# Kernel optimization log

Measured on AMD Instinct MI355X. Metric: run time of the kernel, lower is better.

## Reference

```python
import jax, jax.numpy as jnp
import numpy as np

EMBED_DIM = 1024
N_HEADS = 16
HEAD_DIM = EMBED_DIM // N_HEADS  # 64
ROPE_DIM = 4
N_FREQ = HEAD_DIM // (2 * ROPE_DIM)  # 8 rotary freqs per coordinate axis
ROPE_THETA = 10000.0
FFN_DIM = 4 * EMBED_DIM
N_TOK = 4096
N_SEQ = 8
EPS = 1e-5
NEG_INF = -1e30


def setup_inputs() -> dict:
    key = jax.random.key(0)
    ks = jax.random.split(key, 16)
    s = 0.02
    coords = jax.random.uniform(ks[0], (N_TOK, ROPE_DIM), jnp.float32) * 10.0
    feats = jax.random.normal(ks[1], (N_TOK, EMBED_DIM), jnp.float32)
    interior = jnp.sort(jax.random.randint(ks[2], (N_SEQ - 1,), 1, N_TOK)).astype(jnp.int32)
    cu_seqlens = jnp.concatenate([jnp.zeros((1,), jnp.int32), interior,
                                  jnp.full((1,), N_TOK, jnp.int32)])
    # learnable RoPE inverse frequencies, one bank per coordinate axis
    base = 1.0 / (ROPE_THETA ** (jnp.arange(N_FREQ, dtype=jnp.float32) * 2.0 * ROPE_DIM / HEAD_DIM))
    inv_freq = jnp.tile(base[None, :], (ROPE_DIM, 1))  # [rope_dim, n_freq]
    return {
        "coords": coords,
        "feats": feats,
        "cu_seqlens": cu_seqlens,
        "Wqkv": jax.random.normal(ks[3], (EMBED_DIM, 3 * EMBED_DIM), jnp.float32) * s,
        "bqkv": jnp.zeros((3 * EMBED_DIM,), jnp.float32),
        "Wo": jax.random.normal(ks[4], (EMBED_DIM, EMBED_DIM), jnp.float32) * s,
        "bo": jnp.zeros((EMBED_DIM,), jnp.float32),
        "inv_freq": inv_freq,
        "ln1_g": jnp.ones((EMBED_DIM,), jnp.float32),
        "ln1_b": jnp.zeros((EMBED_DIM,), jnp.float32),
        "W1": jax.random.normal(ks[5], (EMBED_DIM, FFN_DIM), jnp.float32) * s,
        "b1": jnp.zeros((FFN_DIM,), jnp.float32),
        "W2": jax.random.normal(ks[6], (FFN_DIM, EMBED_DIM), jnp.float32) * s,
        "b2": jnp.zeros((EMBED_DIM,), jnp.float32),
        "ln2_g": jnp.ones((EMBED_DIM,), jnp.float32),
        "ln2_b": jnp.zeros((EMBED_DIM,), jnp.float32),
    }


def _layernorm(x, g, b):
    mu = jnp.mean(x, axis=-1, keepdims=True)
    xc = x - mu
    var = jnp.mean(xc * xc, axis=-1, keepdims=True)
    return xc * jax.lax.rsqrt(var + EPS) * g + b


def _block_forward(coords, feats, cu_seqlens, Wqkv, bqkv, Wo, bo, inv_freq,
                   ln1_g, ln1_b, W1, b1, W2, b2, ln2_g, ln2_b):
    N, D = feats.shape
    qkv = (feats @ Wqkv + bqkv).reshape(N, 3, N_HEADS, HEAD_DIM)
    q, k, v = qkv[:, 0], qkv[:, 1], qkv[:, 2]  # each [N, H, hd]

    # multi-dimensional learnable RoPE: each coord axis rotates its freq bank
    ang = jnp.einsum('nd,df->ndf', coords, inv_freq).reshape(N, 1, HEAD_DIM // 2)
    cos, sin = jnp.cos(ang), jnp.sin(ang)

    def rot(x):
        x1, x2 = jnp.split(x, 2, axis=-1)
        return jnp.concatenate([x1 * cos - x2 * sin, x2 * cos + x1 * sin], axis=-1)

    q, k = rot(q), rot(k)

    # varlen block-diagonal attention mask from cu_seqlens
    seg = jnp.searchsorted(cu_seqlens[1:], jnp.arange(N), side='right')
    mask = seg[:, None] == seg[None, :]  # [N, N]

    scores = jnp.einsum('nhd,mhd->hnm', q, k) / np.sqrt(HEAD_DIM).astype(np.float32)
    scores = jnp.where(mask[None, :, :], scores, NEG_INF)
    attn = jax.nn.softmax(scores, axis=-1)
    o = jnp.einsum('hnm,mhd->nhd', attn, v).reshape(N, D) @ Wo + bo

    h = _layernorm(feats + o, ln1_g, ln1_b)
    f = jax.nn.gelu(h @ W1 + b1) @ W2 + b2
    return _layernorm(h + f, ln2_g, ln2_b)


def reference(coords, feats, cu_seqlens, Wqkv, bqkv, Wo, bo, inv_freq,
              ln1_g, ln1_b, W1, b1, W2, b2, ln2_g, ln2_b):
    return _block_forward(coords, feats, cu_seqlens, Wqkv, bqkv, Wo, bo, inv_freq,
                          ln1_g, ln1_b, W1, b1, W2, b2, ln2_g, ln2_b)
```

## Files before the change

### kernel.cpp

```cpp
#include <hip/hip_runtime.h>

#define NTOK 4096
#define EMB  1024
#define NH   16
#define HD   64
#define FFN  4096

typedef __bf16 bf16x8 __attribute__((ext_vector_type(8)));
typedef float  f32x4  __attribute__((ext_vector_type(4)));

#define ASG __attribute__((address_space(1)))
#define ASL __attribute__((address_space(3)))

__device__ __forceinline__ float b2f(unsigned short u) {
    union { unsigned int i; float f; } v; v.i = ((unsigned int)u) << 16; return v.f;
}
__device__ __forceinline__ unsigned short f2b(float f) {
    return __builtin_bit_cast(unsigned short, (__bf16)f);
}
__device__ __forceinline__ float ldf(const void* p, size_t i, int f32) {
    return f32 ? ((const float*)p)[i] : b2f(((const unsigned short*)p)[i]);
}
__device__ __forceinline__ int probe_f32(const void* p) {
    return ((const unsigned int*)p)[0] == 0x3F800000u ? 1 : 0;
}
__device__ __forceinline__ float gelu_f(float x) {
    float z = 0.7978845608028654f * (x + 0.044715f * x * x * x);
    float t = 1.0f - 2.0f / (__expf(2.0f * z) + 1.0f);
    return 0.5f * x * (1.0f + t);
}
__device__ __forceinline__ void gll16(const void* g, void* l) {
    __builtin_amdgcn_global_load_lds((const ASG void*)g, (ASL void*)l, 16, 0, 0);
}

__global__ __launch_bounds__(256) void convert_kernel(
    const void* __restrict__ feats, const void* __restrict__ bqkv,
    const void* __restrict__ bo, const void* __restrict__ b1,
    const void* __restrict__ b2, const void* __restrict__ g1,
    const void* __restrict__ e1, const void* __restrict__ g2,
    const void* __restrict__ e2, const int* __restrict__ cu,
    unsigned short* __restrict__ feats_bf, unsigned short* __restrict__ smalls,
    int* __restrict__ seg, const void* __restrict__ pr) {
    const int f32 = probe_f32(pr);
    int bid = blockIdx.x, tid = threadIdx.x;
    if (bid < 4096) {
        size_t base = (size_t)bid * 1024 + tid * 4;
        union { unsigned short u[4]; int2 v; } U;
#pragma unroll
        for (int i = 0; i < 4; ++i) U.u[i] = f2b(ldf(feats, base + i, f32));
        *reinterpret_cast<int2*>(&feats_bf[base]) = U.v;
    } else if (bid < 4109) {
        int flat = (bid - 4096) * 1024 + tid * 4;
        const void* src; int off;
        if      (flat < 3072)  { src = bqkv; off = 0; }
        else if (flat < 4096)  { src = bo;   off = 3072; }
        else if (flat < 8192)  { src = b1;   off = 4096; }
        else if (flat < 9216)  { src = b2;   off = 8192; }
        else if (flat < 10240) { src = g1;   off = 9216; }
        else if (flat < 11264) { src = e1;   off = 10240; }
        else if (flat < 12288) { src = g2;   off = 11264; }
        else                   { src = e2;   off = 12288; }
        union { unsigned short u[4]; int2 v; } U;
#pragma unroll
        for (int i = 0; i < 4; ++i) U.u[i] = f2b(ldf(src, flat - off + i, f32));
        *reinterpret_cast<int2*>(&smalls[flat]) = U.v;
    } else {
        int n = (bid - 4109) * 256 + tid;
        int s = 0;
#pragma unroll
        for (int i = 1; i <= 8; ++i) s += (cu[i] <= n) ? 1 : 0;
        seg[n] = s;
    }
}

__global__ __launch_bounds__(64) void sched_kernel(
    const int* __restrict__ seg, const int* __restrict__ cu,
    int* __restrict__ perm) {
    __shared__ int w[64];
    int t = threadIdx.x;
    int s0 = seg[t * 64], s1 = seg[t * 64 + 63];
    int kb = cu[s0] & ~63;
    int kend = cu[s1 + 1];
    w[t] = (kend - kb + 63) >> 6;
    __syncthreads();
    int wt = w[t], r = 0;
#pragma unroll
    for (int j = 0; j < 64; ++j) {
        int wj = w[j];
        r += (wj > wt || (wj == wt && j < t)) ? 1 : 0;
    }
    perm[r] = t;
}

__global__ __launch_bounds__(256) void transpose_kernel(
    const void* __restrict__ W, unsigned short* __restrict__ O,
    int K, int N, const void* __restrict__ pr) {
    const int f32 = probe_f32(pr);
    int b = blockIdx.x, tid = threadIdx.x;
    int ntiles = N >> 6;
    int nt = b % ntiles, kt = b / ntiles;
    __shared__ unsigned short T[64][66];
    int cx = (tid & 15) * 4, ry = tid >> 4;
#pragma unroll
    for (int i = 0; i < 4; ++i) {
        int k = kt * 64 + ry + 16 * i;
        size_t base = (size_t)k * N + nt * 64 + cx;
#pragma unroll
        for (int j = 0; j < 4; ++j)
            T[ry + 16 * i][cx + j] = f2b(ldf(W, base + j, f32));
    }
    __syncthreads();
#pragma unroll
    for (int i = 0; i < 4; ++i) {
        int n = nt * 64 + ry + 16 * i;
        union { unsigned short u[4]; int2 v; } U;
#pragma unroll
        for (int j = 0; j < 4; ++j) U.u[j] = T[cx + j][ry + 16 * i];
        *reinterpret_cast<int2*>(&O[(size_t)n * K + kt * 64 + cx]) = U.v;
    }
}

template <int ACT, int OUTEXT, int TN, int SPLITV, int SPLITK>
__global__ __launch_bounds__(256) void gemm128(
    const unsigned short* __restrict__ A, const unsigned short* __restrict__ Bt,
    const unsigned short* __restrict__ bias, void* __restrict__ C,
    void* __restrict__ C2,
    int M, int N, int K, int lda, int ldb, const void* __restrict__ pr) {
    constexpr int NB = TN / 32;
    __shared__ __align__(16) unsigned short As[128 * 64];
    __shared__ __align__(16) unsigned short Bs[TN * 64];
    const int f32 = OUTEXT ? probe_f32(pr) : 0;
    const int tid = threadIdx.x;
    const int wave = tid >> 6, lane = tid & 63;
    const int wy = wave >> 1, wx = wave & 1;
    const int qm = lane & 15, quad = lane >> 4;
    const int z = SPLITK ? (int)blockIdx.z : 0;
    int bx, by;
    if ((gridDim.y & 7) == 0) {
        int lin = blockIdx.y * gridDim.x + blockIdx.x;
        int ypg = gridDim.y >> 3;
        int xcd = lin & 7, s = lin >> 3;
        int sy = s / gridDim.x;
        by = xcd * ypg + sy;
        bx = s - sy * gridDim.x;
    } else { bx = blockIdx.x; by = blockIdx.y; }
    const int m0 = by * 128, n0 = bx * TN;
    const int r = lane >> 3, gl = lane & 7;

    f32x4 acc[4][NB];
#pragma unroll
    for (int i = 0; i < 4; ++i)
#pragma unroll
        for (int j = 0; j < NB; ++j) acc[i][j] = (f32x4){0.f, 0.f, 0.f, 0.f};

    const int koff = SPLITK ? z * K : 0;
    const unsigned short* Ab = A  + (size_t)m0 * lda + koff;
    const unsigned short* Bb = Bt + (size_t)n0 * ldb + koff;

    for (int k0 = 0; k0 < K; k0 += 64) {
#pragma unroll
        for (int i = 0; i < 4; ++i) {
            int cc = wave * 4 + i;
            gll16(Ab + (size_t)(8 * cc + r) * lda + k0 + ((gl ^ r) << 3), &As[cc * 512]);
        }
#pragma unroll
        for (int i = 0; i < NB; ++i) {
            int cc = wave * NB + i;
            gll16(Bb + (size_t)(8 * cc + r) * ldb + k0 + ((gl ^ r) << 3), &Bs[cc * 512]);
        }
        __syncthreads();
#pragma unroll
        for (int h = 0; h < 2; ++h) {
            bf16x8 af[4], bfr[NB];
#pragma unroll
            for (int i = 0; i < 4; ++i) {
                int phys = (((h * 4 + quad) ^ (qm & 7)) << 3);
                af[i] = *reinterpret_cast<const bf16x8*>(&As[(64 * wy + 16 * i + qm) * 64 + phys]);
            }
#pragma unroll
            for (int j = 0; j < NB; ++j) {
                int phys = (((h * 4 + quad) ^ (qm & 7)) << 3);
                bfr[j] = *reinterpret_cast<const bf16x8*>(&Bs[((TN / 2) * wx + 16 * j + qm) * 64 + phys]);
            }
#pragma unroll
            for (int i = 0; i < 4; ++i)
#pragma unroll
                for (int j = 0; j < NB; ++j)
                    acc[i][j] = __builtin_amdgcn_mfma_f32_16x16x32_bf16(af[i], bfr[j], acc[i][j], 0, 0, 0);
        }
        __syncthreads();
    }
#pragma unroll
    for (int j = 0; j < NB; ++j) {
        int col = n0 + (TN / 2) * wx + 16 * j + qm;
        float bv = (SPLITK && z) ? 0.f : b2f(bias[col]);
        if (SPLITV && n0 >= 2048) {
            int d = col - 2048;
#pragma unroll
            for (int i = 0; i < 4; ++i) {
                int rowb = m0 + 64 * wy + 16 * i + quad * 4;
                union { unsigned short u[4]; int2 v; } U;
#pragma unroll
                for (int rr = 0; rr < 4; ++rr) U.u[rr] = f2b(acc[i][j][rr] + bv);
                *reinterpret_cast<int2*>((unsigned short*)C2 + (size_t)d * 4096 + rowb) = U.v;
            }
        } else {
            const int ldc = SPLITV ? 2048 : N;
            void* Cz = (SPLITK && z) ? C2 : C;
#pragma unroll
            for (int i = 0; i < 4; ++i) {
                int rowb = m0 + 64 * wy + 16 * i + quad * 4;
#pragma unroll
                for (int rr = 0; rr < 4; ++rr) {
                    size_t idx = (size_t)(rowb + rr) * ldc + col;
                    float v = acc[i][j][rr] + bv;
                    if (ACT == 1) v = gelu_f(v);
                    if (OUTEXT && f32) ((float*)Cz)[idx] = v;
                    else               ((unsigned short*)Cz)[idx] = f2b(v);
                }
            }
        }
    }
}

__global__ __launch_bounds__(256) void rope_kernel(
    const void* __restrict__ coords, const void* __restrict__ inv_freq,
    unsigned short* __restrict__ qk, const void* __restrict__ pr) {
    const int f32 = probe_f32(pr);
    int n = blockIdx.x, tid = threadIdx.x;
#pragma unroll
    for (int it = 0; it < 2; ++it) {
        int idx = tid + it * 256;
        int hh = idx >> 5, f = idx & 31;
        float c  = ldf(coords, n * 4 + (f >> 3), f32);
        float iv = ldf(inv_freq, f, f32);
        float sn, cs;
        sincosf(c * iv, &sn, &cs);
#pragma unroll
        for (int w = 0; w < 2; ++w) {
            size_t base = (size_t)n * 2048 + (size_t)w * 1024 + hh * 64;
            float scl = w ? 1.0f : 0.125f;
            float x1 = b2f(qk[base + f]);
            float x2 = b2f(qk[base + 32 + f]);
            qk[base + f]      = f2b((x1 * cs - x2 * sn) * scl);
            qk[base + 32 + f] = f2b((x2 * cs + x1 * sn) * scl);
        }
    }
}

__global__ __launch_bounds__(256) void attn_part(
    const unsigned short* __restrict__ qk, const unsigned short* __restrict__ vt,
    const int* __restrict__ seg, const int* __restrict__ cu,
    const int* __restrict__ perm,
    unsigned short* __restrict__ u0, unsigned short* __restrict__ u1,
    unsigned short* __restrict__ u2, float* __restrict__ ml) {
    const int h = blockIdx.x / 3;
    const int piece = blockIdx.x - 3 * h;
    const int t3 = perm[blockIdx.y];
    const int t0 = t3 * 64;
    const int tid  = threadIdx.x;
    const int wave = tid >> 6, lane = tid & 63;
    const int qm = lane & 15, quad = lane >> 4;

    __shared__ __align__(16) unsigned short Ks[2][64][64];
    __shared__ __align__(16) unsigned short Vs[2][80][64];
    __shared__ __align__(16) unsigned short Ps[64][64];
    __shared__ int segq[64], segk[2][64];

    const unsigned short* qrow = qk + (size_t)(t0 + 16 * wave + qm) * 2048 + h * 64;
    bf16x8 af0 = *reinterpret_cast<const bf16x8*>(qrow + quad * 8);
    bf16x8 af1 = *reinterpret_cast<const bf16x8*>(qrow + 32 + quad * 8);

    {
        int rr = tid >> 4, cc = (tid & 15) * 4;
        unsigned short val = (rr == 0) ? (unsigned short)0x3F80 : (unsigned short)0;
#pragma unroll
        for (int b = 0; b < 2; ++b)
#pragma unroll
            for (int j = 0; j < 4; ++j) Vs[b][64 + rr][cc + j] = val;
    }
    if (tid < 64) segq[tid] = seg[t0 + tid];
    __syncthreads();

    const int kbegA = cu[segq[0]] & ~63;
    const int kendT = cu[segq[63] + 1];
    const int nchunks = (kendT - kbegA + 63) >> 6;
    const int third = (nchunks + 2) / 3;
    const int kb = kbegA + piece * third * 64;
    const int ke = min(kendT, kbegA + (piece + 1) * third * 64);

    int sqr[4];
#pragma unroll
    for (int r = 0; r < 4; ++r) sqr[r] = segq[16 * wave + quad * 4 + r];
    const int wsmin = segq[16 * wave];
    const int wsmax = segq[16 * wave + 15];

    float m[4];
    f32x4 o[5];
#pragma unroll
    for (int r = 0; r < 4; ++r) m[r] = -1e30f;
#pragma unroll
    for (int t = 0; t < 5; ++t) o[t] = (f32x4){0.f, 0.f, 0.f, 0.f};

    const int krow = tid >> 2, kdc = (tid & 3) * 16;
    const int k7 = krow & 7;
    const int sw0 = (((tid & 3) * 2) ^ k7) << 3;
    const int sw1 = ((((tid & 3) * 2 + 1)) ^ k7) << 3;
    const int rsw0 = (quad ^ (qm & 7)) << 3;
    const int rsw1 = ((quad + 4) ^ (qm & 7)) << 3;
    int4 kA, kB, vA, vB; int sg;
#define LOAD_CHUNK(KC)                                                                   \
    {                                                                                    \
        const unsigned short* kp = qk + (size_t)((KC) + krow) * 2048 + 1024 + h * 64 + kdc; \
        kA = *reinterpret_cast<const int4*>(kp);                                         \
        kB = *reinterpret_cast<const int4*>(kp + 8);                                     \
        const unsigned short* vp = vt + (size_t)(h * 64 + krow) * 4096 + (KC) + kdc;     \
        vA = *reinterpret_cast<const int4*>(vp);                                         \
        vB = *reinterpret_cast<const int4*>(vp + 8);                                     \
        sg = 127;                                                                        \
        if (tid < 64 && (KC) + tid < ke) sg = seg[(KC) + tid];                           \
    }
#define STORE_CHUNK(B)                                                                   \
    {                                                                                    \
        *reinterpret_cast<int4*>(&Ks[B][krow][sw0]) = kA;                                \
        *reinterpret_cast<int4*>(&Ks[B][krow][sw1]) = kB;                                \
        *reinterpret_cast<int4*>(&Vs[B][krow][sw0]) = vA;                                \
        *reinterpret_cast<int4*>(&Vs[B][krow][sw1]) = vB;                                \
        if (tid < 64) segk[B][tid] = sg;                                                 \
    }

    int cur = 0;
    if (kb < ke) {
        LOAD_CHUNK(kb);
        STORE_CHUNK(0);
    }

    for (int kc = kb; kc < ke; kc += 64) {
        const bool have_next = (kc + 64 < ke);
        if (have_next) LOAD_CHUNK(kc + 64);
        __syncthreads();

        const int skmin = segk[cur][0], skmax = segk[cur][63];
        const bool act = !(skmax < wsmin || skmin > wsmax);

        if (act) {
            f32x4 sc[4];
#pragma unroll
            for (int nb = 0; nb < 4; ++nb) {
                bf16x8 bf0 = *reinterpret_cast<const bf16x8*>(&Ks[cur][16 * nb + qm][rsw0]);
                bf16x8 bf1 = *reinterpret_cast<const bf16x8*>(&Ks[cur][16 * nb + qm][rsw1]);
                f32x4 s = (f32x4){0.f, 0.f, 0.f, 0.f};
                s = __builtin_amdgcn_mfma_f32_16x16x32_bf16(af0, bf0, s, 0, 0, 0);
                s = __builtin_amdgcn_mfma_f32_16x16x32_bf16(af1, bf1, s, 0, 0, 0);
                sc[nb] = s;
            }
            if (!((skmin == skmax) & (wsmin == wsmax))) {
#pragma unroll
                for (int nb = 0; nb < 4; ++nb) {
                    int sk = segk[cur][16 * nb + qm];
#pragma unroll
                    for (int r = 0; r < 4; ++r)
                        sc[nb][r] = (sk == sqr[r]) ? sc[nb][r] : -1e30f;
                }
            }
            float alpha[4];
#pragma unroll
            for (int r = 0; r < 4; ++r) {
                float v = fmaxf(fmaxf(sc[0][r], sc[1][r]), fmaxf(sc[2][r], sc[3][r]));
                v = fmaxf(v, __shfl_xor(v, 1, 64));
                v = fmaxf(v, __shfl_xor(v, 2, 64));
                v = fmaxf(v, __shfl_xor(v, 4, 64));
                v = fmaxf(v, __shfl_xor(v, 8, 64));
                float mn = fmaxf(m[r], v);
                alpha[r] = __expf(m[r] - mn);
                m[r] = mn;
            }
#pragma unroll
            for (int nb = 0; nb < 4; ++nb) {
                int R7 = (quad * 4) & 7;
#pragma unroll
                for (int r = 0; r < 4; ++r) {
                    float p = __expf(sc[nb][r] - m[r]);
                    int row = 16 * wave + quad * 4 + r;
                    int phys = (((2 * nb + (qm >> 3)) ^ ((quad * 4 + r) & 7)) << 3) + (qm & 7);
                    Ps[row][phys] = f2b(p);
                }
                (void)R7;
            }
#pragma unroll
            for (int t = 0; t < 5; ++t)
#pragma unroll
                for (int r = 0; r < 4; ++r) o[t][r] *= alpha[r];

            bf16x8 pa0 = *reinterpret_cast<const bf16x8*>(&Ps[16 * wave + qm][rsw0]);
            bf16x8 pa1 = *reinterpret_cast<const bf16x8*>(&Ps[16 * wave + qm][rsw1]);
#pragma unroll
            for (int dt = 0; dt < 4; ++dt) {
                bf16x8 vb0 = *reinterpret_cast<const bf16x8*>(&Vs[cur][16 * dt + qm][rsw0]);
                bf16x8 vb1 = *reinterpret_cast<const bf16x8*>(&Vs[cur][16 * dt + qm][rsw1]);
                o[dt] = __builtin_amdgcn_mfma_f32_16x16x32_bf16(pa0, vb0, o[dt], 0, 0, 0);
                o[dt] = __builtin_amdgcn_mfma_f32_16x16x32_bf16(pa1, vb1, o[dt], 0, 0, 0);
            }
            {
                bf16x8 vb0 = *reinterpret_cast<const bf16x8*>(&Vs[cur][64 + qm][rsw0]);
                bf16x8 vb1 = *reinterpret_cast<const bf16x8*>(&Vs[cur][64 + qm][rsw1]);
                o[4] = __builtin_amdgcn_mfma_f32_16x16x32_bf16(pa0, vb0, o[4], 0, 0, 0);
                o[4] = __builtin_amdgcn_mfma_f32_16x16x32_bf16(pa1, vb1, o[4], 0, 0, 0);
            }
        }
        if (have_next) {
            STORE_CHUNK(cur ^ 1);
        }
        cur ^= 1;
    }
#undef LOAD_CHUNK
#undef STORE_CHUNK
    unsigned short* dst = (piece == 0) ? u0 : ((piece == 1) ? u1 : u2);
#pragma unroll
    for (int dt = 0; dt < 4; ++dt)
#pragma unroll
        for (int r = 0; r < 4; ++r) {
            int row = t0 + 16 * wave + quad * 4 + r;
            dst[(size_t)row * 1024 + h * 64 + 16 * dt + qm] = f2b(o[dt][r]);
        }
    if (qm == 0) {
        float2* ML = (float2*)ml;
#pragma unroll
        for (int r = 0; r < 4; ++r) {
            int row = t0 + 16 * wave + quad * 4 + r;
            ML[((piece * 16 + h) << 12) + row] = make_float2(m[r], o[4][r]);
        }
    }
}

__global__ __launch_bounds__(256) void combine_kernel(
    const unsigned short* __restrict__ u1, const unsigned short* __restrict__ u2,
    const float* __restrict__ ml, unsigned short* __restrict__ u0out) {
    int n = blockIdx.x, tid = threadIdx.x;
    int d4 = tid * 4, h = tid >> 4;
    const float2* ML = (const float2*)ml;
    float2 p0 = ML[(h << 12) + n];
    float2 p1 = ML[((16 + h) << 12) + n];
    float2 p2 = ML[((32 + h) << 12) + n];
    float M = fmaxf(p0.x, fmaxf(p1.x, p2.x));
    float a0 = __expf(p0.x - M), a1 = __expf(p1.x - M), a2 = __expf(p2.x - M);
    float rcp = 1.0f / (a0 * p0.y + a1 * p1.y + a2 * p2.y);
    size_t ix = (size_t)n * 1024 + d4;
    union { int2 q; unsigned short u[4]; } A, B, Cq, R;
    A.q  = *reinterpret_cast<const int2*>(u0out + ix);
    B.q  = *reinterpret_cast<const int2*>(u1 + ix);
    Cq.q = *reinterpret_cast<const int2*>(u2 + ix);
#pragma unroll
    for (int i = 0; i < 4; ++i)
        R.u[i] = f2b((a0 * b2f(A.u[i]) + a1 * b2f(B.u[i]) + a2 * b2f(Cq.u[i])) * rcp);
    *reinterpret_cast<int2*>(u0out + ix) = R.q;
}

template <int OUTEXT>
__global__ __launch_bounds__(256) void ln3_kernel(
    const unsigned short* __restrict__ x1, const unsigned short* __restrict__ x2a,
    const unsigned short* __restrict__ x2b,
    const unsigned short* __restrict__ g, const unsigned short* __restrict__ b,
    void* __restrict__ out, const void* __restrict__ pr) {
    const int f32 = probe_f32(pr);
    int n = blockIdx.x, tid = threadIdx.x;
    __shared__ float red[8];
    const int d0 = tid * 4;
    const size_t ix0 = (size_t)n * EMB + d0;
    float v[4];
    {
        union { int2 q; unsigned short u[4]; } A, Ba, Bb2;
        A.q   = *reinterpret_cast<const int2*>(&x1[ix0]);
        Ba.q  = *reinterpret_cast<const int2*>(&x2a[ix0]);
        Bb2.q = *reinterpret_cast<const int2*>(&x2b[ix0]);
#pragma unroll
        for (int i = 0; i < 4; ++i)
            v[i] = b2f(A.u[i]) + b2f(Ba.u[i]) + b2f(Bb2.u[i]);
    }
    float s = v[0] + v[1] + v[2] + v[3];
#pragma unroll
    for (int off = 1; off < 64; off <<= 1) s += __shfl_xor(s, off, 64);
    if ((tid & 63) == 0) red[tid >> 6] = s;
    __syncthreads();
    float mu = (red[0] + red[1] + red[2] + red[3]) * (1.0f / 1024.0f);
    float sq = 0.0f;
#pragma unroll
    for (int i = 0; i < 4; ++i) { float c = v[i] - mu; sq += c * c; }
#pragma unroll
    for (int off = 1; off < 64; off <<= 1) sq += __shfl_xor(sq, off, 64);
    if ((tid & 63) == 0) red[4 + (tid >> 6)] = sq;
    __syncthreads();
    float var = (red[4] + red[5] + red[6] + red[7]) * (1.0f / 1024.0f);
    float rcp = rsqrtf(var + 1e-5f);
    union { int2 q; unsigned short u[4]; } G, Bb;
    G.q  = *reinterpret_cast<const int2*>(&g[d0]);
    Bb.q = *reinterpret_cast<const int2*>(&b[d0]);
    if (OUTEXT && f32) {
        float4 R;
        R.x = (v[0] - mu) * rcp * b2f(G.u[0]) + b2f(Bb.u[0]);
        R.y = (v[1] - mu) * rcp * b2f(G.u[1]) + b2f(Bb.u[1]);
        R.z = (v[2] - mu) * rcp * b2f(G.u[2]) + b2f(Bb.u[2]);
        R.w = (v[3] - mu) * rcp * b2f(G.u[3]) + b2f(Bb.u[3]);
        *reinterpret_cast<float4*>((float*)out + ix0) = R;
    } else {
        union { int2 q; unsigned short u[4]; } R;
#pragma unroll
        for (int i = 0; i < 4; ++i)
            R.u[i] = f2b((v[i] - mu) * rcp * b2f(G.u[i]) + b2f(Bb.u[i]));
        *reinterpret_cast<int2*>((unsigned short*)out + ix0) = R.q;
    }
}

extern "C" void kernel_launch(void* const* d_in, const int* in_sizes, int n_in,
                              void* d_out, int out_size, void* d_ws, size_t ws_size,
                              hipStream_t stream) {
    const void* coords   = d_in[0];
    const void* feats    = d_in[1];
    const int*  cu       = (const int*)d_in[2];
    const void* Wqkv     = d_in[3];
    const void* bqkv     = d_in[4];
    const void* Wo       = d_in[5];
    const void* bo       = d_in[6];
    const void* inv_freq = d_in[7];
    const void* ln1_g    = d_in[8];
    const void* ln1_b    = d_in[9];
    const void* W1       = d_in[10];
    const void* b1       = d_in[11];
    const void* W2       = d_in[12];
    const void* b2       = d_in[13];
    const void* ln2_g    = d_in[14];
    const void* ln2_b    = d_in[15];
    const void* pr = ln1_g;

    char* ws = (char*)d_ws;
    int* seg = (int*)ws;
    unsigned short* smalls   = (unsigned short*)(ws + 16384);
    unsigned short* bqkv_bf  = smalls;
    unsigned short* bo_bf    = smalls + 3072;
    unsigned short* b1_bf    = smalls + 4096;
    unsigned short* b2_bf    = smalls + 8192;
    unsigned short* g1_bf    = smalls + 9216;
    unsigned short* e1_bf    = smalls + 10240;
    unsigned short* g2_bf    = smalls + 11264;
    unsigned short* e2_bf    = smalls + 12288;
    int* perm                = (int*)(ws + 49152);
    unsigned short* feats_bf = (unsigned short*)(ws + 65536);
    unsigned short* hbuf     = feats_bf;
    unsigned short* W1_t     = (unsigned short*)(ws + 8454144);
    unsigned short* u1buf    = (unsigned short*)(ws + 16842752);
    unsigned short* Wqkv_t   = (unsigned short*)(ws + 18939904);
    unsigned short* qkbuf    = (unsigned short*)(ws + 25231360);
    unsigned short* vtbuf    = (unsigned short*)(ws + 42008576);
    unsigned short* attn_o   = (unsigned short*)(ws + 50397184);
    unsigned short* Wo_t     = (unsigned short*)(ws + 18939904);
    unsigned short* woP0     = (unsigned short*)(ws + 25231360);
    unsigned short* woP1     = (unsigned short*)(ws + 33619968);
    unsigned short* f1       = (unsigned short*)(ws + 25231360);
    unsigned short* ffP0     = (unsigned short*)(ws + 8454144);
    unsigned short* ffP1     = (unsigned short*)(ws + 16842752);
    float* mlbuf = (float*)d_out;
    unsigned short* u2buf = (unsigned short*)((char*)d_out + 2097152);
    unsigned short* W2_t  = (unsigned short*)((char*)d_out + 8388608);

    hipLaunchKernelGGL(convert_kernel, dim3(4125), dim3(256), 0, stream,
                       feats, bqkv, bo, b1, b2, ln1_g, ln1_b, ln2_g, ln2_b, cu,
                       feats_bf, smalls, seg, pr);
    hipLaunchKernelGGL(sched_kernel, dim3(1), dim3(64), 0, stream,
                       seg, cu, perm);
    hipLaunchKernelGGL(transpose_kernel, dim3(768), dim3(256), 0, stream,
                       Wqkv, Wqkv_t, 1024, 3072, pr);
    hipLaunchKernelGGL(transpose_kernel, dim3(1024), dim3(256), 0, stream,
                       W1, W1_t, 1024, 4096, pr);
    hipLaunchKernelGGL((gemm128<0, 0, 128, 1, 0>), dim3(24, 32), dim3(256), 0, stream,
                       feats_bf, Wqkv_t, bqkv_bf, qkbuf, vtbuf, NTOK, 3072, 1024, 1024, 1024, pr);
    hipLaunchKernelGGL(rope_kernel, dim3(NTOK), dim3(256), 0, stream,
                       coords, inv_freq, qkbuf, pr);
    hipLaunchKernelGGL(attn_part, dim3(48, 64), dim3(256), 0, stream,
                       qkbuf, vtbuf, seg, cu, perm, attn_o, u1buf, u2buf, mlbuf);
    hipLaunchKernelGGL(combine_kernel, dim3(NTOK), dim3(256), 0, stream,
                       u1buf, u2buf, mlbuf, attn_o);
    hipLaunchKernelGGL(transpose_kernel, dim3(256), dim3(256), 0, stream,
                       Wo, Wo_t, 1024, 1024, pr);
    hipLaunchKernelGGL((gemm128<0, 0, 128, 0, 1>), dim3(8, 32, 2), dim3(256), 0, stream,
                       attn_o, Wo_t, bo_bf, woP0, woP1, NTOK, 1024, 512, 1024, 1024, pr);
    hipLaunchKernelGGL(transpose_kernel, dim3(1024), dim3(256), 0, stream,
                       W2, W2_t, 4096, 1024, pr);
    hipLaunchKernelGGL((ln3_kernel<0>), dim3(NTOK), dim3(256), 0, stream,
                       feats_bf, woP0, woP1, g1_bf, e1_bf, hbuf, pr);
    hipLaunchKernelGGL((gemm128<1, 0, 128, 0, 0>), dim3(32, 32), dim3(256), 0, stream,
                       hbuf, W1_t, b1_bf, f1, nullptr, NTOK, 4096, 1024, 1024, 1024, pr);
    hipLaunchKernelGGL((gemm128<0, 0, 128, 0, 1>), dim3(8, 32, 2), dim3(256), 0, stream,
                       f1, W2_t, b2_bf, ffP0, ffP1, NTOK, 1024, 2048, 4096, 4096, pr);
    hipLaunchKernelGGL((ln3_kernel<1>), dim3(NTOK), dim3(256), 0, stream,
                       hbuf, ffP0, ffP1, g2_bf, e2_bf, d_out, pr);
}
```

Baseline: 388.0 us.

## Add dedicated 256x256-tile pipelined GEMM for FFN1 with GELU epilogue

Replaces the generic 128-tile GEMM for the first FFN projection with a specialised 512-thread kernel using 256x256 output tiles, double-buffered LDS staging via global-to-LDS loads interleaved across four sub-phases, and XCD-aware block remapping. The larger tile raises arithmetic intensity and data reuse per LDS load, and the interleaved staging aims to overlap memory traffic with MFMA work. It uses many barriers and a large register footprint (128 accumulator floats per thread), which may limit occupancy. It also removes an unused variable in the attention kernel.

```diff
diff --git a/kernel.cpp b/kernel.cpp
--- a/kernel.cpp
+++ b/kernel.cpp
@@ -223,6 +223,117 @@
     }
 }
 
+__global__ __launch_bounds__(512, 2) void gemm256_ffn1(
+    const unsigned short* __restrict__ A, const unsigned short* __restrict__ Bt,
+    const unsigned short* __restrict__ bias, unsigned short* __restrict__ C) {
+    __shared__ __align__(16) unsigned short L[2][2][256][64];
+    const int tid = threadIdx.x;
+    const int wv = tid >> 6, lane = tid & 63;
+    const int wm = wv >> 2, wn = wv & 3;
+    const int qm = lane & 15, quad = lane >> 4;
+    const int r8 = lane >> 3, gl = lane & 7;
+    const int xsw = (gl ^ r8) << 3;
+    int lin = blockIdx.y * 16 + blockIdx.x;
+    int xcd = lin & 7, s = lin >> 3;
+    int by = xcd * 2 + (s >> 4), bx = s & 15;
+    const int m0 = by * 256, n0 = bx * 256;
+    const unsigned short* Ab = A  + (size_t)m0 * 1024;
+    const unsigned short* Bb = Bt + (size_t)n0 * 1024;
+
+    f32x4 acc[8][4];
+#pragma unroll
+    for (int i = 0; i < 8; ++i)
+#pragma unroll
+        for (int j = 0; j < 4; ++j) acc[i][j] = (f32x4){0.f, 0.f, 0.f, 0.f};
+    bf16x8 af[4], bf[4];
+
+#define STG(buf, ten, sl, kn)                                                      \
+    gll16(((ten) ? Bb : Ab) + (size_t)(64 * (sl) + 8 * wv + r8) * 1024 + (kn) + xsw, \
+          &L[buf][ten][64 * (sl) + 8 * wv][0])
+#define RD(mh, h)                                                                  \
+    {                                                                              \
+        const int phys = ((((h) * 4) + quad) ^ (qm & 7)) << 3;                     \
+        _Pragma("unroll")                                                          \
+        for (int i = 0; i < 4; ++i)                                                \
+            af[i] = *reinterpret_cast<const bf16x8*>(                              \
+                &Ac[(wm * 128 + (mh) * 64 + i * 16 + qm) * 64 + phys]);            \
+        _Pragma("unroll")                                                          \
+        for (int j = 0; j < 4; ++j)                                                \
+            bf[j] = *reinterpret_cast<const bf16x8*>(                              \
+                &Bc[(wn * 64 + j * 16 + qm) * 64 + phys]);                         \
+    }
+#define MM(mh, h)                                                                  \
+    _Pragma("unroll")                                                              \
+    for (int i = 0; i < 4; ++i)                                                    \
+        _Pragma("unroll")                                                          \
+        for (int j = 0; j < 4; ++j)                                                \
+            acc[(mh) * 4 + i][j] = __builtin_amdgcn_mfma_f32_16x16x32_bf16(        \
+                af[i], bf[j], acc[(mh) * 4 + i][j], 0, 0, 0);
+
+    STG(0, 0, 0, 0); STG(0, 0, 2, 0);
+    STG(0, 1, 0, 0); STG(0, 1, 1, 0); STG(0, 1, 2, 0); STG(0, 1, 3, 0);
+    STG(0, 0, 1, 0); STG(0, 0, 3, 0);
+    asm volatile("s_waitcnt vmcnt(2)" ::: "memory");
+    __builtin_amdgcn_s_barrier();
+
+    for (int t = 0; t < 16; ++t) {
+        const unsigned short* Ac = &L[t & 1][0][0][0];
+        const unsigned short* Bc = &L[t & 1][1][0][0];
+        const int nb = (t + 1) & 1;
+        const int kn = (t + 1) << 6;
+        const bool more = t < 15;
+        RD(0, 0);
+        if (more) { STG(nb, 0, 0, kn); STG(nb, 0, 2, kn); }
+        __builtin_amdgcn_s_barrier();
+        asm volatile("s_waitcnt lgkmcnt(0)" ::: "memory");
+        __builtin_amdgcn_s_setprio(1); MM(0, 0); __builtin_amdgcn_s_setprio(0);
+        __builtin_amdgcn_s_barrier();
+        RD(0, 1);
+        if (more) {
+            STG(nb, 1, 0, kn); STG(nb, 1, 1, kn);
+            asm volatile("s_waitcnt vmcnt(4)" ::: "memory");
+        } else {
+            asm volatile("s_waitcnt vmcnt(0)" ::: "memory");
+        }
+        __builtin_amdgcn_s_barrier();
+        asm volatile("s_waitcnt lgkmcnt(0)" ::: "memory");
+        __builtin_amdgcn_s_setprio(1); MM(0, 1); __builtin_amdgcn_s_setprio(0);
+        __builtin_amdgcn_s_barrier();
+        RD(1, 0);
+        if (more) { STG(nb, 1, 2, kn); STG(nb, 1, 3, kn); }
+        __builtin_amdgcn_s_barrier();
+        asm volatile("s_waitcnt lgkmcnt(0)" ::: "memory");
+        __builtin_amdgcn_s_setprio(1); MM(1, 0); __builtin_amdgcn_s_setprio(0);
+        __builtin_amdgcn_s_barrier();
+        RD(1, 1);
+        if (more) {
+            STG(nb, 0, 1, kn); STG(nb, 0, 3, kn);
+            asm volatile("s_waitcnt vmcnt(2)" ::: "memory");
+        }
+        __builtin_amdgcn_s_barrier();
+        asm volatile("s_waitcnt lgkmcnt(0)" ::: "memory");
+        __builtin_amdgcn_s_setprio(1); MM(1, 1); __builtin_amdgcn_s_setprio(0);
+        __builtin_amdgcn_s_barrier();
+    }
+#undef STG
+#undef RD
+#undef MM
+#pragma unroll
+    for (int j = 0; j < 4; ++j) {
+        int col = n0 + wn * 64 + j * 16 + qm;
+        float bv = b2f(bias[col]);
+#pragma unroll
+        for (int i = 0; i < 8; ++i) {
+            int rowb = m0 + wm * 128 + i * 16 + quad * 4;
+#pragma unroll
+            for (int rr = 0; rr < 4; ++rr) {
+                float v = gelu_f(acc[i][j][rr] + bv);
+                C[(size_t)(rowb + rr) * 4096 + col] = f2b(v);
+            }
+        }
+    }
+}
+
 __global__ __launch_bounds__(256) void rope_kernel(
     const void* __restrict__ coords, const void* __restrict__ inv_freq,
     unsigned short* __restrict__ qk, const void* __restrict__ pr) {
@@ -377,7 +488,6 @@
             }
 #pragma unroll
             for (int nb = 0; nb < 4; ++nb) {
-                int R7 = (quad * 4) & 7;
 #pragma unroll
                 for (int r = 0; r < 4; ++r) {
                     float p = __expf(sc[nb][r] - m[r]);
@@ -385,7 +495,6 @@
                     int phys = (((2 * nb + (qm >> 3)) ^ ((quad * 4 + r) & 7)) << 3) + (qm & 7);
                     Ps[row][phys] = f2b(p);
                 }
-                (void)R7;
             }
 #pragma unroll
             for (int t = 0; t < 5; ++t)
@@ -587,8 +696,8 @@
                        W2, W2_t, 4096, 1024, pr);
     hipLaunchKernelGGL((ln3_kernel<0>), dim3(NTOK), dim3(256), 0, stream,
                        feats_bf, woP0, woP1, g1_bf, e1_bf, hbuf, pr);
-    hipLaunchKernelGGL((gemm128<1, 0, 128, 0, 0>), dim3(32, 32), dim3(256), 0, stream,
-                       hbuf, W1_t, b1_bf, f1, nullptr, NTOK, 4096, 1024, 1024, 1024, pr);
+    hipLaunchKernelGGL(gemm256_ffn1, dim3(16, 16), dim3(512), 0, stream,
+                       hbuf, W1_t, b1_bf, f1);
     hipLaunchKernelGGL((gemm128<0, 0, 128, 0, 1>), dim3(8, 32, 2), dim3(256), 0, stream,
                        f1, W2_t, b2_bf, ffP0, ffP1, NTOK, 1024, 2048, 4096, 4096, pr);
     hipLaunchKernelGGL((ln3_kernel<1>), dim3(NTOK), dim3(256), 0, stream,
```

After: 378.3 us. 2.5% less time.
